# Performance work log

Hardware: AMD Instinct MI355X
Metric: run time of the kernel (lower is better)

## Reference

```python
import jax, jax.numpy as jnp
import numpy as np

B, D = 16, 8192
CH = 32
N_BLOCKS = 24
DILATIONS = [2 ** i for i in range(8)] * 3  # 3 stacks of 8 layers


def _causal_conv(x, W, b, dilation):
    # x: (B, Cin, L); W: (Cout, Cin, K). Causal = left-pad (K-1)*dilation only,
    # which equals torch's symmetric-pad-then-slice-right trick.
    pad = (W.shape[-1] - 1) * dilation
    y = jax.lax.conv_general_dilated(
        x, W, window_strides=(1,), padding=[(pad, 0)],
        rhs_dilation=(dilation,), dimension_numbers=('NCH', 'OIH', 'NCH'))
    return y + b[None, :, None]


def setup_inputs() -> dict:
    key = jax.random.key(0)
    ks = jax.random.split(key, 13)
    s = 0.1  # keep activations in a sane range
    return {
        'x': jax.random.normal(ks[0], (B, D), jnp.float32),
        'W0': jax.random.normal(ks[1], (CH, 1, 2), jnp.float32) * s,
        'b0': jax.random.normal(ks[2], (CH,), jnp.float32) * s,
        'Wd': jax.random.normal(ks[3], (N_BLOCKS, 2 * CH, CH, 2), jnp.float32) * s,
        'bd': jax.random.normal(ks[4], (N_BLOCKS, 2 * CH), jnp.float32) * s,
        'W1': jax.random.normal(ks[5], (N_BLOCKS, CH, CH), jnp.float32) * s,
        'b1': jax.random.normal(ks[6], (N_BLOCKS, CH), jnp.float32) * s,
        'Wf': jax.random.normal(ks[7], (CH, CH), jnp.float32) * s,
        'bf': jax.random.normal(ks[8], (CH,), jnp.float32) * s,
        'fW1': jax.random.normal(ks[9], (64, CH * 4), jnp.float32) * s,
        'fb1': jax.random.normal(ks[10], (64,), jnp.float32) * s,
        'fW2': jax.random.normal(ks[11], (10, 64), jnp.float32) * s,
        'fb2': jax.random.normal(ks[12], (10,), jnp.float32) * s,
    }


def reference(x, W0, b0, Wd, bd, W1, b1, Wf, bf, fW1, fb1, fW2, fb2):
    h = _causal_conv(x[:, None, :], W0, b0, 1)  # (B, 32, L)
    skip_sum = jnp.zeros_like(h)
    for i, dil in enumerate(DILATIONS):
        z = _causal_conv(h, Wd[i], bd[i], dil)          # (B, 64, L)
        f, g = jnp.split(z, 2, axis=1)
        gated = jnp.tanh(f) * jax.nn.sigmoid(g)          # (B, 32, L)
        skip = jnp.einsum('oc,bcl->bol', W1[i], gated) + b1[i][None, :, None]
        h = h + skip                                     # residual (dropout = eval identity)
        skip_sum = skip_sum + skip                       # sum of stacked skips
    y = jax.nn.relu(skip_sum)
    y = jnp.einsum('oc,bcl->bol', Wf, y) + bf[None, :, None]
    y = jax.nn.relu(y)
    # AdaptiveMaxPool1d(4): L divisible by 4 -> max over contiguous chunks
    Bc, C, L = y.shape
    y = y.reshape(Bc, C, 4, L // 4).max(axis=-1)         # (B, 32, 4)
    y = y.reshape(Bc, C * 4)
    y = jax.nn.relu(y @ fW1.T + fb1)
    return y @ fW2.T + fb2
```

## Files before the change

### kernel.cpp

```cpp
#include <hip/hip_runtime.h>
#include <hip/hip_bf16.h>

#define BATCH 16
#define SEQ 8192
#define CH 32
#define NB 24

typedef __attribute__((ext_vector_type(8))) short short8;
typedef __attribute__((ext_vector_type(4))) float f32x4;

#define LROW 36

__device__ __forceinline__ unsigned short f2bf(float x) {
    __hip_bfloat16 b = __float2bfloat16(x);
    unsigned short u;
    __builtin_memcpy(&u, &b, 2);
    return u;
}
__device__ __forceinline__ float bf2f(unsigned short h) {
    return __uint_as_float(((unsigned int)h) << 16);
}
__device__ __forceinline__ float rcp_fast(float x) { return __builtin_amdgcn_rcpf(x); }

__device__ __forceinline__ float gate_fn(float f, float g) {
    float ef = __expf(-2.0f * fabsf(f));
    float eg = __expf(-g);
    float num = 1.0f - ef;
    float den = (1.0f + ef) * (1.0f + eg);
    return copysignf(num * rcp_fast(den), f);
}

__device__ __forceinline__ void split2(float v, unsigned short& h, unsigned short& l) {
    h = f2bf(v);
    l = f2bf(v - bf2f(h));
}

__global__ __launch_bounds__(256) void k_prep(const float* __restrict__ Wd,
                                              const float* __restrict__ bd,
                                              const float* __restrict__ W1,
                                              const float* __restrict__ b1,
                                              unsigned short* __restrict__ stream,
                                              float* __restrict__ pooled) {
    int i = blockIdx.x;
    int tid = threadIdx.x;
    int l = tid & 63, q4 = tid >> 6;
    int p = l & 15, h4 = l >> 4;
    const float* wd  = Wd + (size_t)i * 64 * 64;
    const float* w1  = W1 + (size_t)i * 1024;
    const float* bdp = bd + (size_t)i * 64;
    const float* b1p = b1 + (size_t)i * 32;
    unsigned short* out = stream + (size_t)i * (28672 / 2);

    for (int g = blockIdx.x * 256 + tid; g < BATCH * CH * 4; g += NB * 256)
        pooled[g] = 0.0f;

    {
        int rt = q4;
        int is_g = (rt >= 2) ? 32 : 0;
        int ch = 8 * (p >> 2) + 4 * (rt & 1) + (p & 3);
        int row = ch + is_g;
        for (int q = 0; q < 2; ++q) {
            int slot = rt * 2 + q;
            for (int j = 0; j < 8; ++j) {
                int k = 32 * q + 8 * h4 + j;
                int c = k & 31, tap = k >> 5;
                float w = wd[row * 64 + c * 2 + tap];
                unsigned short hi = f2bf(w);
                out[(size_t)slot * 512 + l * 8 + j] = hi;
                out[(size_t)(8 + slot) * 512 + l * 8 + j] = f2bf(w - bf2f(hi));
            }
        }
    }
    if (q4 < 2) {
        int rt2 = q4;
        for (int j = 0; j < 8; ++j) {
            int o = 16 * rt2 + p, c = 8 * h4 + j;
            float w = w1[o * 32 + c];
            unsigned short hi = f2bf(w);
            out[(size_t)(16 + rt2) * 512 + l * 8 + j] = hi;
            out[(size_t)(18 + rt2) * 512 + l * 8 + j] = f2bf(w - bf2f(hi));
        }
    }
    float* outf = (float*)stream + (size_t)i * (28672 / 4);
    if (q4 == 2) {
        for (int rt = 0; rt < 4; ++rt) {
            int is_g = (rt >= 2) ? 32 : 0;
            for (int r = 0; r < 4; ++r)
                outf[(size_t)(20 + rt) * 256 + l * 4 + r] =
                    bdp[8 * h4 + 4 * (rt & 1) + r + is_g];
        }
    }
    if (q4 == 3) {
        for (int rt2 = 0; rt2 < 2; ++rt2)
            for (int r = 0; r < 4; ++r)
                outf[(size_t)(24 + rt2) * 256 + l * 4 + r] = b1p[16 * rt2 + 4 * h4 + r];
    }
}

__global__ __launch_bounds__(512, 2) void k_stack(
        const float* __restrict__ hin,
        float* __restrict__ hout,
        const float* __restrict__ x,
        const float* __restrict__ W0,
        const float* __restrict__ b0,
        const float* __restrict__ Wf,
        const float* __restrict__ bf,
        float* __restrict__ pooled,
        const unsigned short* __restrict__ wstream,
        int stack) {
    __shared__ __align__(16) float lh[768 * LROW];
    __shared__ float red[8 * CH];

    int tid = threadIdx.x;
    int lane = tid & 63, wave = tid >> 6;
    int p = lane & 15, h4 = lane >> 4;
    int bb = blockIdx.x >> 4;
    int T0 = (blockIdx.x & 15) * 512;
    bool first = (stack == 0);
    bool last  = (stack == 2);

    const float* pin = hin + (size_t)bb * SEQ * CH;
    float* pout = hout + (size_t)bb * SEQ * CH;
    const float* px = x + (size_t)bb * SEQ;

    const f32x4 zero4 = {0.0f, 0.0f, 0.0f, 0.0f};

    if (first) {
        for (int i = tid; i < 768; i += 512) {
            int t = T0 - 256 + i;
            float* dst = &lh[i * LROW];
            if (t >= 0) {
                float xt = px[t];
                float xm = (t > 0) ? px[t - 1] : 0.0f;
                __align__(16) float hv[CH];
#pragma unroll
                for (int c = 0; c < CH; ++c)
                    hv[c] = W0[c * 2] * xm + W0[c * 2 + 1] * xt + b0[c];
#pragma unroll
                for (int k = 0; k < 8; ++k)
                    *(f32x4*)(dst + 4 * k) = *(const f32x4*)(hv + 4 * k);
            } else {
#pragma unroll
                for (int k = 0; k < 8; ++k)
                    *(f32x4*)(dst + 4 * k) = zero4;
            }
        }
    } else {
        for (int i = tid; i < 768; i += 512) {
            int t = T0 - 256 + i;
            float* dst = &lh[i * LROW];
            if (t >= 0) {
                const float* src = pin + (size_t)t * CH;
#pragma unroll
                for (int k = 0; k < 8; ++k)
                    *(f32x4*)(dst + 4 * k) = *(const f32x4*)(src + 4 * k);
            } else {
#pragma unroll
                for (int k = 0; k < 8; ++k)
                    *(f32x4*)(dst + 4 * k) = zero4;
            }
        }
    }
    __syncthreads();

#pragma unroll 1
    for (int l = 0; l < 8; ++l) {
        int dil = 1 << l;
        const unsigned short* frag = wstream + (size_t)(8 * stack + l) * 14336;
        const short8* fs = (const short8*)frag;
        short8 Ah[4][2], Al[4][2], Sh[2], Sl[2];
#pragma unroll
        for (int rt = 0; rt < 4; ++rt)
#pragma unroll
            for (int q = 0; q < 2; ++q) {
                Ah[rt][q] = fs[(rt * 2 + q) * 64 + lane];
                Al[rt][q] = fs[(8 + rt * 2 + q) * 64 + lane];
            }
#pragma unroll
        for (int rt2 = 0; rt2 < 2; ++rt2) {
            Sh[rt2] = fs[(16 + rt2) * 64 + lane];
            Sl[rt2] = fs[(18 + rt2) * 64 + lane];
        }
        const f32x4* ff = (const f32x4*)frag;
        f32x4 bFG[4], bS[2];
#pragma unroll
        for (int rt = 0; rt < 4; ++rt) bFG[rt] = ff[(20 + rt) * 64 + lane];
#pragma unroll
        for (int rt2 = 0; rt2 < 2; ++rt2) bS[rt2] = ff[(24 + rt2) * 64 + lane];

        f32x4 hnew[6][2];

#pragma unroll
        for (int s6 = 0; s6 < 6; ++s6) {
            int tpos = wave * 96 + s6 * 16 + p;
            int tq = tpos - dil;
            bool ok = (T0 - 256 + tq >= 0);
            int tqc = (tq > 0) ? tq : 0;

            const float* r1 = &lh[tpos * LROW + 8 * h4];
            const float* r0 = &lh[tqc * LROW + 8 * h4];
            f32x4 v1a = *(const f32x4*)r1, v1b = *(const f32x4*)(r1 + 4);
            f32x4 v0a = *(const f32x4*)r0, v0b = *(const f32x4*)(r0 + 4);
            if (!ok) { v0a = zero4; v0b = zero4; }
            short8 bh1, bl1, bh0, bl0;
#pragma unroll
            for (int j = 0; j < 4; ++j) {
                unsigned short hh, ll;
                split2(v1a[j], hh, ll); bh1[j] = (short)hh; bl1[j] = (short)ll;
                split2(v1b[j], hh, ll); bh1[4 + j] = (short)hh; bl1[4 + j] = (short)ll;
                split2(v0a[j], hh, ll); bh0[j] = (short)hh; bl0[j] = (short)ll;
                split2(v0b[j], hh, ll); bh0[4 + j] = (short)hh; bl0[4 + j] = (short)ll;
            }

            f32x4 acc[4];
#pragma unroll
            for (int rt = 0; rt < 4; ++rt) {
                f32x4 a = bFG[rt];
                a = __builtin_amdgcn_mfma_f32_16x16x32_bf16(Ah[rt][0], bh0, a, 0, 0, 0);
                a = __builtin_amdgcn_mfma_f32_16x16x32_bf16(Ah[rt][1], bh1, a, 0, 0, 0);
                a = __builtin_amdgcn_mfma_f32_16x16x32_bf16(Ah[rt][0], bl0, a, 0, 0, 0);
                a = __builtin_amdgcn_mfma_f32_16x16x32_bf16(Ah[rt][1], bl1, a, 0, 0, 0);
                a = __builtin_amdgcn_mfma_f32_16x16x32_bf16(Al[rt][0], bh0, a, 0, 0, 0);
                a = __builtin_amdgcn_mfma_f32_16x16x32_bf16(Al[rt][1], bh1, a, 0, 0, 0);
                acc[rt] = a;
            }

            short8 Bgh, Bgl;
#pragma unroll
            for (int rt = 0; rt < 2; ++rt)
#pragma unroll
                for (int r = 0; r < 4; ++r) {
                    float gated = gate_fn(acc[rt][r], acc[rt + 2][r]);
                    unsigned short hh, ll;
                    split2(gated, hh, ll);
                    Bgh[4 * rt + r] = (short)hh;
                    Bgl[4 * rt + r] = (short)ll;
                }

            f32x4 sacc[2];
#pragma unroll
            for (int rt2 = 0; rt2 < 2; ++rt2) {
                f32x4 a = bS[rt2];
                a = __builtin_amdgcn_mfma_f32_16x16x32_bf16(Sh[rt2], Bgh, a, 0, 0, 0);
                a = __builtin_amdgcn_mfma_f32_16x16x32_bf16(Sh[rt2], Bgl, a, 0, 0, 0);
                a = __builtin_amdgcn_mfma_f32_16x16x32_bf16(Sl[rt2], Bgh, a, 0, 0, 0);
                sacc[rt2] = a;
            }

#pragma unroll
            for (int rt2 = 0; rt2 < 2; ++rt2) {
                f32x4 hold = *(const f32x4*)&lh[tpos * LROW + 16 * rt2 + 4 * h4];
                hnew[s6][rt2] = hold + sacc[rt2];
            }
        }
        __syncthreads();

#pragma unroll
        for (int s6 = 0; s6 < 6; ++s6) {
            int tpos = wave * 96 + s6 * 16 + p;
#pragma unroll
            for (int rt2 = 0; rt2 < 2; ++rt2)
                *(f32x4*)&lh[tpos * LROW + 16 * rt2 + 4 * h4] = hnew[s6][rt2];
        }
        __syncthreads();
    }

    if (!last) {
        int i = 256 + tid;
        int t = T0 + tid;
        const float* src = &lh[i * LROW];
        float* dst = pout + (size_t)t * CH;
#pragma unroll
        for (int k = 0; k < 8; ++k)
            *(f32x4*)(dst + 4 * k) = *(const f32x4*)(src + 4 * k);
    } else {
        int i = 256 + tid;
        int t = T0 + tid;
        int q = (blockIdx.x & 15) >> 2;
        float xt = px[t];
        float xm = (t > 0) ? px[t - 1] : 0.0f;
        const float* src = &lh[i * LROW];

        float r[CH];
#pragma unroll
        for (int c = 0; c < CH; ++c) {
            float h0 = W0[c * 2] * xm + W0[c * 2 + 1] * xt + b0[c];
            r[c] = fmaxf(src[c] - h0, 0.0f);
        }
        float y[CH];
#pragma unroll 1
        for (int o = 0; o < CH; ++o) {
            const float* w = Wf + o * CH;
            float a0 = bf[o], a1 = 0.0f, a2 = 0.0f, a3 = 0.0f;
#pragma unroll
            for (int c = 0; c < CH; c += 4) {
                a0 += w[c + 0] * r[c + 0];
                a1 += w[c + 1] * r[c + 1];
                a2 += w[c + 2] * r[c + 2];
                a3 += w[c + 3] * r[c + 3];
            }
            y[o] = fmaxf((a0 + a1) + (a2 + a3), 0.0f);
        }
#pragma unroll
        for (int o = 0; o < CH; ++o) {
#pragma unroll
            for (int off = 32; off >= 1; off >>= 1)
                y[o] = fmaxf(y[o], __shfl_xor(y[o], off));
        }
        if (lane == 0) {
#pragma unroll
            for (int o = 0; o < CH; ++o) red[wave * CH + o] = y[o];
        }
        __syncthreads();
        if (tid < CH) {
            float m = red[tid];
#pragma unroll
            for (int w8 = 1; w8 < 8; ++w8) m = fmaxf(m, red[w8 * CH + tid]);
            atomicMax((unsigned int*)&pooled[bb * (CH * 4) + tid * 4 + q],
                      __float_as_uint(m));
        }
    }
}

__global__ __launch_bounds__(1024) void k_final2(const float* __restrict__ pooled,
                                                 const float* __restrict__ fW1,
                                                 const float* __restrict__ fb1,
                                                 const float* __restrict__ fW2,
                                                 const float* __restrict__ fb2,
                                                 float* __restrict__ out) {
    __shared__ float y1[BATCH * 64];
    int tid = threadIdx.x;
    int b = tid >> 6, o = tid & 63;
    float acc = fb1[o];
#pragma unroll
    for (int j = 0; j < 128; ++j) acc += fW1[o * 128 + j] * pooled[b * 128 + j];
    y1[b * 64 + o] = fmaxf(acc, 0.0f);
    __syncthreads();
    if (tid < BATCH * 10) {
        int bb = tid / 10, o2 = tid % 10;
        float a2 = fb2[o2];
#pragma unroll
        for (int j = 0; j < 64; ++j) a2 += fW2[o2 * 64 + j] * y1[bb * 64 + j];
        out[bb * 10 + o2] = a2;
    }
}

extern "C" void kernel_launch(void* const* d_in, const int* in_sizes, int n_in,
                              void* d_out, int out_size, void* d_ws, size_t ws_size,
                              hipStream_t stream) {
    const float* x   = (const float*)d_in[0];
    const float* W0  = (const float*)d_in[1];
    const float* b0  = (const float*)d_in[2];
    const float* Wd  = (const float*)d_in[3];
    const float* bd  = (const float*)d_in[4];
    const float* W1  = (const float*)d_in[5];
    const float* b1  = (const float*)d_in[6];
    const float* Wf  = (const float*)d_in[7];
    const float* bf  = (const float*)d_in[8];
    const float* fW1 = (const float*)d_in[9];
    const float* fb1 = (const float*)d_in[10];
    const float* fW2 = (const float*)d_in[11];
    const float* fb2 = (const float*)d_in[12];
    float* out = (float*)d_out;

    const size_t HS = (size_t)BATCH * SEQ * CH;
    float* bufA = (float*)d_ws;
    float* bufB = bufA + HS;
    unsigned short* wstream = (unsigned short*)(bufB + HS);
    float* pooled = (float*)(wstream + (size_t)NB * 14336);

    k_prep<<<NB, 256, 0, stream>>>(Wd, bd, W1, b1, wstream, pooled);

    k_stack<<<256, 512, 0, stream>>>(bufA, bufB, x, W0, b0, Wf, bf, pooled, wstream, 0);
    k_stack<<<256, 512, 0, stream>>>(bufB, bufA, x, W0, b0, Wf, bf, pooled, wstream, 1);
    k_stack<<<256, 512, 0, stream>>>(bufA, bufA, x, W0, b0, Wf, bf, pooled, wstream, 2);

    k_final2<<<1, 1024, 0, stream>>>(pooled, fW1, fb1, fW2, fb2, out);
}
```

Measured before the change: 338.5 us.

## Store hidden state as pre-split bf16 hi/lo planes and halve tile size

The residual state in LDS and in global memory now lives as separate bf16 hi and lo planes instead of fp32. The MFMA B operands can then be loaded directly with no per-use split, and the split happens once, when the state is written back. The time tile shrinks from 512 to 256 outputs per block, with 512 blocks and occupancy raised to 4 blocks per CU. That cuts LDS use but raises the share of recomputed halo from one third to one half. Holding h as a hi+lo sum each layer may slightly change numerics versus fp32.

```diff
diff --git a/kernel.cpp b/kernel.cpp
--- a/kernel.cpp
+++ b/kernel.cpp
@@ -7,9 +7,8 @@
 #define NB 24
 
 typedef __attribute__((ext_vector_type(8))) short short8;
+typedef __attribute__((ext_vector_type(4))) short short4v;
 typedef __attribute__((ext_vector_type(4))) float f32x4;
-
-#define LROW 36
 
 __device__ __forceinline__ unsigned short f2bf(float x) {
     __hip_bfloat16 b = __float2bfloat16(x);
@@ -97,9 +96,11 @@
     }
 }
 
-__global__ __launch_bounds__(512, 2) void k_stack(
-        const float* __restrict__ hin,
-        float* __restrict__ hout,
+__global__ __launch_bounds__(512, 4) void k_stack(
+        const unsigned short* __restrict__ hin_hi,
+        const unsigned short* __restrict__ hin_lo,
+        unsigned short* __restrict__ hout_hi,
+        unsigned short* __restrict__ hout_lo,
         const float* __restrict__ x,
         const float* __restrict__ W0,
         const float* __restrict__ b0,
@@ -108,56 +109,62 @@
         float* __restrict__ pooled,
         const unsigned short* __restrict__ wstream,
         int stack) {
-    __shared__ __align__(16) float lh[768 * LROW];
-    __shared__ float red[8 * CH];
+    __shared__ __align__(16) unsigned short lhi[512][40];
+    __shared__ __align__(16) unsigned short llo[512][40];
 
     int tid = threadIdx.x;
     int lane = tid & 63, wave = tid >> 6;
     int p = lane & 15, h4 = lane >> 4;
-    int bb = blockIdx.x >> 4;
-    int T0 = (blockIdx.x & 15) * 512;
+    int bb = blockIdx.x >> 5;
+    int T0 = (blockIdx.x & 31) * 256;
     bool first = (stack == 0);
     bool last  = (stack == 2);
 
-    const float* pin = hin + (size_t)bb * SEQ * CH;
-    float* pout = hout + (size_t)bb * SEQ * CH;
+    const unsigned short* pin_hi = hin_hi + (size_t)bb * SEQ * CH;
+    const unsigned short* pin_lo = hin_lo + (size_t)bb * SEQ * CH;
+    unsigned short* pout_hi = hout_hi + (size_t)bb * SEQ * CH;
+    unsigned short* pout_lo = hout_lo + (size_t)bb * SEQ * CH;
     const float* px = x + (size_t)bb * SEQ;
 
-    const f32x4 zero4 = {0.0f, 0.0f, 0.0f, 0.0f};
-
-    if (first) {
-        for (int i = tid; i < 768; i += 512) {
-            int t = T0 - 256 + i;
-            float* dst = &lh[i * LROW];
+    const short8 zero8 = {0, 0, 0, 0, 0, 0, 0, 0};
+
+    {
+        int i = tid;
+        int t = T0 - 256 + i;
+        if (first) {
             if (t >= 0) {
                 float xt = px[t];
                 float xm = (t > 0) ? px[t - 1] : 0.0f;
-                __align__(16) float hv[CH];
-#pragma unroll
-                for (int c = 0; c < CH; ++c)
-                    hv[c] = W0[c * 2] * xm + W0[c * 2 + 1] * xt + b0[c];
-#pragma unroll
-                for (int k = 0; k < 8; ++k)
-                    *(f32x4*)(dst + 4 * k) = *(const f32x4*)(hv + 4 * k);
+#pragma unroll
+                for (int c = 0; c < CH; ++c) {
+                    float v = W0[c * 2] * xm + W0[c * 2 + 1] * xt + b0[c];
+                    unsigned short hh, ll;
+                    split2(v, hh, ll);
+                    lhi[i][c] = hh;
+                    llo[i][c] = ll;
+                }
             } else {
 #pragma unroll
-                for (int k = 0; k < 8; ++k)
-                    *(f32x4*)(dst + 4 * k) = zero4;
-            }
-        }
-    } else {
-        for (int i = tid; i < 768; i += 512) {
-            int t = T0 - 256 + i;
-            float* dst = &lh[i * LROW];
+                for (int k = 0; k < 4; ++k) {
+                    *(short8*)&lhi[i][8 * k] = zero8;
+                    *(short8*)&llo[i][8 * k] = zero8;
+                }
+            }
+        } else {
             if (t >= 0) {
-                const float* src = pin + (size_t)t * CH;
-#pragma unroll
-                for (int k = 0; k < 8; ++k)
-                    *(f32x4*)(dst + 4 * k) = *(const f32x4*)(src + 4 * k);
+                const unsigned short* sh = pin_hi + (size_t)t * CH;
+                const unsigned short* sl = pin_lo + (size_t)t * CH;
+#pragma unroll
+                for (int k = 0; k < 4; ++k) {
+                    *(short8*)&lhi[i][8 * k] = *(const short8*)(sh + 8 * k);
+                    *(short8*)&llo[i][8 * k] = *(const short8*)(sl + 8 * k);
+                }
             } else {
 #pragma unroll
-                for (int k = 0; k < 8; ++k)
-                    *(f32x4*)(dst + 4 * k) = zero4;
+                for (int k = 0; k < 4; ++k) {
+                    *(short8*)&lhi[i][8 * k] = zero8;
+                    *(short8*)&llo[i][8 * k] = zero8;
+                }
             }
         }
     }
@@ -188,29 +195,20 @@
 #pragma unroll
         for (int rt2 = 0; rt2 < 2; ++rt2) bS[rt2] = ff[(24 + rt2) * 64 + lane];
 
-        f32x4 hnew[6][2];
-
-#pragma unroll
-        for (int s6 = 0; s6 < 6; ++s6) {
-            int tpos = wave * 96 + s6 * 16 + p;
+        f32x4 hnew[4][2];
+
+#pragma unroll
+        for (int s6 = 0; s6 < 4; ++s6) {
+            int tpos = wave * 64 + s6 * 16 + p;
             int tq = tpos - dil;
             bool ok = (T0 - 256 + tq >= 0);
             int tqc = (tq > 0) ? tq : 0;
 
-            const float* r1 = &lh[tpos * LROW + 8 * h4];
-            const float* r0 = &lh[tqc * LROW + 8 * h4];
-            f32x4 v1a = *(const f32x4*)r1, v1b = *(const f32x4*)(r1 + 4);
-            f32x4 v0a = *(const f32x4*)r0, v0b = *(const f32x4*)(r0 + 4);
-            if (!ok) { v0a = zero4; v0b = zero4; }
-            short8 bh1, bl1, bh0, bl0;
-#pragma unroll
-            for (int j = 0; j < 4; ++j) {
-                unsigned short hh, ll;
-                split2(v1a[j], hh, ll); bh1[j] = (short)hh; bl1[j] = (short)ll;
-                split2(v1b[j], hh, ll); bh1[4 + j] = (short)hh; bl1[4 + j] = (short)ll;
-                split2(v0a[j], hh, ll); bh0[j] = (short)hh; bl0[j] = (short)ll;
-                split2(v0b[j], hh, ll); bh0[4 + j] = (short)hh; bl0[4 + j] = (short)ll;
-            }
+            short8 bh1 = *(const short8*)&lhi[tpos][8 * h4];
+            short8 bl1 = *(const short8*)&llo[tpos][8 * h4];
+            short8 bh0 = *(const short8*)&lhi[tqc][8 * h4];
+            short8 bl0 = *(const short8*)&llo[tqc][8 * h4];
+            if (!ok) { bh0 = zero8; bl0 = zero8; }
 
             f32x4 acc[4];
 #pragma unroll
@@ -249,73 +247,92 @@
 
 #pragma unroll
             for (int rt2 = 0; rt2 < 2; ++rt2) {
-                f32x4 hold = *(const f32x4*)&lh[tpos * LROW + 16 * rt2 + 4 * h4];
-                hnew[s6][rt2] = hold + sacc[rt2];
+                int ch = 16 * rt2 + 4 * h4;
+                short4v hh = *(const short4v*)&lhi[tpos][ch];
+                short4v hl = *(const short4v*)&llo[tpos][ch];
+                f32x4 hv;
+#pragma unroll
+                for (int r = 0; r < 4; ++r)
+                    hv[r] = bf2f((unsigned short)hh[r]) + bf2f((unsigned short)hl[r]);
+                hnew[s6][rt2] = hv + sacc[rt2];
             }
         }
         __syncthreads();
 
 #pragma unroll
-        for (int s6 = 0; s6 < 6; ++s6) {
-            int tpos = wave * 96 + s6 * 16 + p;
-#pragma unroll
-            for (int rt2 = 0; rt2 < 2; ++rt2)
-                *(f32x4*)&lh[tpos * LROW + 16 * rt2 + 4 * h4] = hnew[s6][rt2];
+        for (int s6 = 0; s6 < 4; ++s6) {
+            int tpos = wave * 64 + s6 * 16 + p;
+#pragma unroll
+            for (int rt2 = 0; rt2 < 2; ++rt2) {
+                __align__(8) unsigned short oh[4], ol[4];
+#pragma unroll
+                for (int r = 0; r < 4; ++r)
+                    split2(hnew[s6][rt2][r], oh[r], ol[r]);
+                int ch = 16 * rt2 + 4 * h4;
+                *(short4v*)&lhi[tpos][ch] = *(const short4v*)oh;
+                *(short4v*)&llo[tpos][ch] = *(const short4v*)ol;
+            }
         }
         __syncthreads();
     }
 
     if (!last) {
-        int i = 256 + tid;
-        int t = T0 + tid;
-        const float* src = &lh[i * LROW];
-        float* dst = pout + (size_t)t * CH;
-#pragma unroll
-        for (int k = 0; k < 8; ++k)
-            *(f32x4*)(dst + 4 * k) = *(const f32x4*)(src + 4 * k);
+        if (tid < 256) {
+            int i = 256 + tid;
+            int t = T0 + tid;
+            unsigned short* dh = pout_hi + (size_t)t * CH;
+            unsigned short* dl = pout_lo + (size_t)t * CH;
+#pragma unroll
+            for (int k = 0; k < 4; ++k) {
+                *(short8*)(dh + 8 * k) = *(const short8*)&lhi[i][8 * k];
+                *(short8*)(dl + 8 * k) = *(const short8*)&llo[i][8 * k];
+            }
+        }
     } else {
-        int i = 256 + tid;
-        int t = T0 + tid;
-        int q = (blockIdx.x & 15) >> 2;
-        float xt = px[t];
-        float xm = (t > 0) ? px[t - 1] : 0.0f;
-        const float* src = &lh[i * LROW];
-
-        float r[CH];
-#pragma unroll
-        for (int c = 0; c < CH; ++c) {
-            float h0 = W0[c * 2] * xm + W0[c * 2 + 1] * xt + b0[c];
-            r[c] = fmaxf(src[c] - h0, 0.0f);
-        }
-        float y[CH];
+        float* red = (float*)&lhi[0][0];
+        int q = (blockIdx.x & 31) >> 3;
+        if (tid < 256) {
+            int i = 256 + tid;
+            int t = T0 + tid;
+            float xt = px[t];
+            float xm = (t > 0) ? px[t - 1] : 0.0f;
+
+            float r[CH];
+#pragma unroll
+            for (int c = 0; c < CH; ++c) {
+                float h0 = W0[c * 2] * xm + W0[c * 2 + 1] * xt + b0[c];
+                float hf = bf2f(lhi[i][c]) + bf2f(llo[i][c]);
+                r[c] = fmaxf(hf - h0, 0.0f);
+            }
+            float y[CH];
 #pragma unroll 1
-        for (int o = 0; o < CH; ++o) {
-            const float* w = Wf + o * CH;
-            float a0 = bf[o], a1 = 0.0f, a2 = 0.0f, a3 = 0.0f;
-#pragma unroll
-            for (int c = 0; c < CH; c += 4) {
-                a0 += w[c + 0] * r[c + 0];
-                a1 += w[c + 1] * r[c + 1];
-                a2 += w[c + 2] * r[c + 2];
-                a3 += w[c + 3] * r[c + 3];
-            }
-            y[o] = fmaxf((a0 + a1) + (a2 + a3), 0.0f);
-        }
-#pragma unroll
-        for (int o = 0; o < CH; ++o) {
-#pragma unroll
-            for (int off = 32; off >= 1; off >>= 1)
-                y[o] = fmaxf(y[o], __shfl_xor(y[o], off));
-        }
-        if (lane == 0) {
-#pragma unroll
-            for (int o = 0; o < CH; ++o) red[wave * CH + o] = y[o];
+            for (int o = 0; o < CH; ++o) {
+                const float* w = Wf + o * CH;
+                float a0 = bf[o], a1 = 0.0f, a2 = 0.0f, a3 = 0.0f;
+#pragma unroll
+                for (int c = 0; c < CH; c += 4) {
+                    a0 += w[c + 0] * r[c + 0];
+                    a1 += w[c + 1] * r[c + 1];
+                    a2 += w[c + 2] * r[c + 2];
+                    a3 += w[c + 3] * r[c + 3];
+                }
+                y[o] = fmaxf((a0 + a1) + (a2 + a3), 0.0f);
+            }
+#pragma unroll
+            for (int o = 0; o < CH; ++o) {
+#pragma unroll
+                for (int off = 32; off >= 1; off >>= 1)
+                    y[o] = fmaxf(y[o], __shfl_xor(y[o], off));
+            }
+            if (lane == 0) {
+#pragma unroll
+                for (int o = 0; o < CH; ++o) red[wave * CH + o] = y[o];
+            }
         }
         __syncthreads();
         if (tid < CH) {
-            float m = red[tid];
-#pragma unroll
-            for (int w8 = 1; w8 < 8; ++w8) m = fmaxf(m, red[w8 * CH + tid]);
+            float m = fmaxf(fmaxf(red[tid], red[CH + tid]),
+                            fmaxf(red[2 * CH + tid], red[3 * CH + tid]));
             atomicMax((unsigned int*)&pooled[bb * (CH * 4) + tid * 4 + q],
                       __float_as_uint(m));
         }
@@ -364,16 +381,21 @@
     float* out = (float*)d_out;
 
     const size_t HS = (size_t)BATCH * SEQ * CH;
-    float* bufA = (float*)d_ws;
-    float* bufB = bufA + HS;
-    unsigned short* wstream = (unsigned short*)(bufB + HS);
+    unsigned short* hiA = (unsigned short*)d_ws;
+    unsigned short* loA = hiA + HS;
+    unsigned short* hiB = loA + HS;
+    unsigned short* loB = hiB + HS;
+    unsigned short* wstream = loB + HS;
     float* pooled = (float*)(wstream + (size_t)NB * 14336);
 
     k_prep<<<NB, 256, 0, stream>>>(Wd, bd, W1, b1, wstream, pooled);
 
-    k_stack<<<256, 512, 0, stream>>>(bufA, bufB, x, W0, b0, Wf, bf, pooled, wstream, 0);
-    k_stack<<<256, 512, 0, stream>>>(bufB, bufA, x, W0, b0, Wf, bf, pooled, wstream, 1);
-    k_stack<<<256, 512, 0, stream>>>(bufA, bufA, x, W0, b0, Wf, bf, pooled, wstream, 2);
+    k_stack<<<512, 512, 0, stream>>>(hiA, loA, hiB, loB, x, W0, b0, Wf, bf,
+                                     pooled, wstream, 0);
+    k_stack<<<512, 512, 0, stream>>>(hiB, loB, hiA, loA, x, W0, b0, Wf, bf,
+                                     pooled, wstream, 1);
+    k_stack<<<512, 512, 0, stream>>>(hiA, loA, hiB, loB, x, W0, b0, Wf, bf,
+                                     pooled, wstream, 2);
 
     k_final2<<<1, 1024, 0, stream>>>(pooled, fW1, fb1, fW2, fb2, out);
 }
```

Result: slower. 447.5 us (+32.2%).
